# Kernel tuning notes

Hardware: AMD Instinct MI355X
Metric: run time of the kernel (lower is better)

## Reference

```python
import jax, jax.numpy as jnp
import numpy as np

N = 50000          # num nodes
E = 800000         # num edges (before self-loops)
F_IN = 128         # num_node_features
HEADS = 8          # num_heads (layer 1)
F_HEAD = 16        # features_per_head
N_CLASSES = 32     # num_classes (layer 2, heads=1)
NEG_SLOPE = 0.2    # PyG GATConv default LeakyReLU slope


def setup_inputs() -> dict:
    key = jax.random.key(0)
    ks = jax.random.split(key, 9)
    x = jax.random.normal(ks[0], (N, F_IN), jnp.float32)
    src = jax.random.randint(ks[1], (E,), 0, N, dtype=jnp.int32)
    dst = jax.random.randint(ks[2], (E,), 0, N, dtype=jnp.int32)
    # layer 1 params
    W1 = jax.random.normal(ks[3], (F_IN, HEADS * F_HEAD), jnp.float32) / np.sqrt(F_IN).astype(np.float32)
    a_src1 = jax.random.normal(ks[4], (HEADS, F_HEAD), jnp.float32) * 0.1
    a_dst1 = jax.random.normal(ks[5], (HEADS, F_HEAD), jnp.float32) * 0.1
    b1 = jnp.zeros((HEADS * F_HEAD,), jnp.float32)  # bias_init = zeros_
    # layer 2 params (heads=1)
    W2 = jax.random.normal(ks[6], (HEADS * F_HEAD, N_CLASSES), jnp.float32) / np.sqrt(HEADS * F_HEAD).astype(np.float32)
    a_src2 = jax.random.normal(ks[7], (1, N_CLASSES), jnp.float32) * 0.1
    a_dst2 = jax.random.normal(ks[8], (1, N_CLASSES), jnp.float32) * 0.1
    b2 = jnp.zeros((N_CLASSES,), jnp.float32)
    return {"x": x, "src": src, "dst": dst,
            "W1": W1, "a_src1": a_src1, "a_dst1": a_dst1, "b1": b1,
            "W2": W2, "a_src2": a_src2, "a_dst2": a_dst2, "b2": b2}


def gat_conv(x, src, dst, W, a_src, a_dst, b, heads, feat):
    """PyG-style GATConv (concat=True, add_self_loops=True)."""
    h = (x @ W).reshape(N, heads, feat)                 # [N,H,F]
    al_src = jnp.sum(h * a_src, axis=-1)                # [N,H]
    al_dst = jnp.sum(h * a_dst, axis=-1)                # [N,H]
    loop = jnp.arange(N, dtype=src.dtype)
    s = jnp.concatenate([src, loop])                    # [E+N]
    d = jnp.concatenate([dst, loop])                    # [E+N]
    e = jax.nn.leaky_relu(al_src[s] + al_dst[d], NEG_SLOPE)   # [E+N,H]
    # numerically stable softmax over edges grouped by dst node
    m = jax.ops.segment_max(e, d, num_segments=N)       # [N,H]
    ex = jnp.exp(e - m[d])
    denom = jax.ops.segment_sum(ex, d, num_segments=N)  # [N,H]
    alpha = ex / denom[d]                               # [E+N,H]
    out = jax.ops.segment_sum(alpha[:, :, None] * h[s], d, num_segments=N)  # [N,H,F]
    return out.reshape(N, heads * feat) + b


def reference(x, src, dst, W1, a_src1, a_dst1, b1, W2, a_src2, a_dst2, b2):
    h = gat_conv(x, src, dst, W1, a_src1, a_dst1, b1, HEADS, F_HEAD)
    h = jax.nn.elu(h)
    h = gat_conv(h, src, dst, W2, a_src2, a_dst2, b2, 1, N_CLASSES)
    return jax.nn.log_softmax(h, axis=1)
```

## Files before the change

kernel.cpp:

```cpp
#include <hip/hip_runtime.h>

#define N_NODES   50000
#define N_EDGES   800000
#define NEG_SLOPE 0.2f
#define NBKT      256
#define NPB       196
#define EPB       3125

__device__ __forceinline__ float leaky(float x) {
    return x > 0.f ? x : x * NEG_SLOPE;
}

__device__ __forceinline__ unsigned short f2bf(float f) {
    unsigned int u = __float_as_uint(f);
    unsigned int r = (u + 0x7FFFu + ((u >> 16) & 1u)) >> 16;
    return (unsigned short)r;
}

__device__ __forceinline__ float2 bf2f2(unsigned int p) {
    return make_float2(__uint_as_float(p << 16),
                       __uint_as_float(p & 0xFFFF0000u));
}

__device__ __forceinline__ void fma4(float4& acc, const float4 a,
                                     const float4 w0, const float4 w1,
                                     const float4 w2, const float4 w3) {
    acc.x = fmaf(a.x, w0.x, fmaf(a.y, w1.x, fmaf(a.z, w2.x, fmaf(a.w, w3.x, acc.x))));
    acc.y = fmaf(a.x, w0.y, fmaf(a.y, w1.y, fmaf(a.z, w2.y, fmaf(a.w, w3.y, acc.y))));
    acc.z = fmaf(a.x, w0.z, fmaf(a.y, w1.z, fmaf(a.z, w2.z, fmaf(a.w, w3.z, acc.z))));
    acc.w = fmaf(a.x, w0.w, fmaf(a.y, w1.w, fmaf(a.z, w2.w, fmaf(a.w, w3.w, acc.w))));
}

__device__ __forceinline__ float dot4(const float4 a, const float4 b) {
    return a.x * b.x + a.y * b.y + a.z * b.z + a.w * b.w;
}

__global__ __launch_bounds__(256) void k_hist(const int* __restrict__ dst,
                                              int* __restrict__ hist_g) {
    __shared__ int h[NBKT];
    const int tid = threadIdx.x, blk = blockIdx.x;
    h[tid] = 0;
    __syncthreads();
    const int e0 = blk * EPB;
    for (int j = e0 + tid; j < e0 + EPB; j += 256)
        atomicAdd(&h[dst[j] / NPB], 1);
    __syncthreads();
    hist_g[tid * NBKT + blk] = h[tid];
}

__global__ __launch_bounds__(256) void k_scanA(const int* __restrict__ hist_g,
                                               int* __restrict__ offs,
                                               int* __restrict__ totals) {
    __shared__ int sc[256];
    const int b = blockIdx.x, tid = threadIdx.x;
    int v = hist_g[b * 256 + tid];
    sc[tid] = v;
    __syncthreads();
    for (int off = 1; off < 256; off <<= 1) {
        int add = (tid >= off) ? sc[tid - off] : 0;
        __syncthreads();
        sc[tid] += add;
        __syncthreads();
    }
    offs[b * 256 + tid] = sc[tid] - v;
    if (tid == 255) totals[b] = sc[255];
}

__global__ __launch_bounds__(256) void k_bin_gemm1(
    const int* __restrict__ src, const int* __restrict__ dst,
    const int* __restrict__ offs, const int* __restrict__ totals,
    unsigned int* __restrict__ binned,
    const float* __restrict__ x, const float* __restrict__ W1,
    const float* __restrict__ a_src, const float* __restrict__ a_dst,
    unsigned short* __restrict__ h1b, float* __restrict__ al_src,
    float* __restrict__ al_dst)
{
    __shared__ __align__(16) unsigned char smem[65536];
    const int tid = threadIdx.x;

    if (blockIdx.x < NBKT) {
        int* cur = (int*)smem;
        int* sc  = (int*)(smem + 1024);
        const int blk = blockIdx.x;
        const int tv = totals[tid];
        sc[tid] = tv;
        __syncthreads();
        for (int off = 1; off < 256; off <<= 1) {
            int add = (tid >= off) ? sc[tid - off] : 0;
            __syncthreads();
            sc[tid] += add;
            __syncthreads();
        }
        cur[tid] = (sc[tid] - tv) + offs[tid * NBKT + blk];
        __syncthreads();
        const int e0 = blk * EPB;
        for (int j = e0 + tid; j < e0 + EPB; j += 256) {
            int d   = dst[j];
            int bkt = d / NPB;
            int dl  = d - bkt * NPB;
            int pos = atomicAdd(&cur[bkt], 1);
            binned[pos] = (unsigned int)src[j] | ((unsigned int)dl << 18);
        }
        return;
    }

    float4* xs4 = (float4*)smem;
    float4* ws4 = (float4*)(smem + 32768);
    const int bid  = (int)blockIdx.x - NBKT;
    const int half = bid & 1;
    const int row0 = (bid >> 1) * 64;
    const int tc   = tid & 15;
    const int tr   = tid >> 4;
    const float4* x4  = (const float4*)x;
    const float4* W14 = (const float4*)W1;

    #pragma unroll
    for (int p = 0; p < 8; ++p) {
        int i = tid + p * 256;
        int k = i >> 4, c4 = i & 15;
        ws4[k * 16 + c4] = W14[k * 32 + half * 16 + c4];
    }
    #pragma unroll
    for (int p = 0; p < 8; ++p) {
        int i = tid + p * 256;
        int r = i >> 5, k4 = i & 31;
        int gr = row0 + r; if (gr > N_NODES - 1) gr = N_NODES - 1;
        xs4[r * 32 + (k4 ^ ((r >> 2) & 7))] = x4[gr * 32 + k4];
    }
    __syncthreads();

    float4 acc[4];
    #pragma unroll
    for (int i = 0; i < 4; ++i) acc[i] = make_float4(0.f, 0.f, 0.f, 0.f);
    const int sw = tr & 7;
    #pragma unroll 2
    for (int k4 = 0; k4 < 32; ++k4) {
        float4 w0 = ws4[(4 * k4 + 0) * 16 + tc];
        float4 w1 = ws4[(4 * k4 + 1) * 16 + tc];
        float4 w2 = ws4[(4 * k4 + 2) * 16 + tc];
        float4 w3 = ws4[(4 * k4 + 3) * 16 + tc];
        const int kk = k4 ^ sw;
        #pragma unroll
        for (int i = 0; i < 4; ++i) {
            float4 a = xs4[(4 * tr + i) * 32 + kk];
            fma4(acc[i], a, w0, w1, w2, w3);
        }
    }

    const int c0   = half * 64 + 4 * tc;
    const int head = c0 >> 4;
    const float4 as4 = ((const float4*)a_src)[half * 16 + tc];
    const float4 ad4 = ((const float4*)a_dst)[half * 16 + tc];
    #pragma unroll
    for (int i = 0; i < 4; ++i) {
        int r = row0 + 4 * tr + i;
        if (r < N_NODES) {
            ((ushort4*)h1b)[r * 32 + half * 16 + tc] =
                make_ushort4(f2bf(acc[i].x), f2bf(acc[i].y),
                             f2bf(acc[i].z), f2bf(acc[i].w));
            float s = dot4(acc[i], as4);
            float d = dot4(acc[i], ad4);
            s += __shfl_xor(s, 1); s += __shfl_xor(s, 2);
            d += __shfl_xor(d, 1); d += __shfl_xor(d, 2);
            if ((tc & 3) == 0) {
                al_src[r * 8 + head] = s;
                al_dst[r * 8 + head] = d;
            }
        }
    }
}

__global__ __launch_bounds__(256) void k_csr_fine(const unsigned int* __restrict__ binned,
                                                  const int* __restrict__ totals,
                                                  int* __restrict__ row_ptr,
                                                  int* __restrict__ csr) {
    __shared__ int cnt[256];
    __shared__ int sc[256];
    __shared__ int cur[256];
    const int b = blockIdx.x, tid = threadIdx.x;
    sc[tid] = totals[tid];
    __syncthreads();
    for (int off = 1; off < 256; off <<= 1) {
        int add = (tid >= off) ? sc[tid - off] : 0;
        __syncthreads();
        sc[tid] += add;
        __syncthreads();
    }
    const int start = (b == 0) ? 0 : sc[b - 1];
    const int end   = sc[b];
    cnt[tid] = 0;
    __syncthreads();
    for (int j = start + tid; j < end; j += 256)
        atomicAdd(&cnt[(binned[j] >> 18) & 255], 1);
    __syncthreads();
    const int v = cnt[tid];
    sc[tid] = v;
    __syncthreads();
    for (int off = 1; off < 256; off <<= 1) {
        int add = (tid >= off) ? sc[tid - off] : 0;
        __syncthreads();
        sc[tid] += add;
        __syncthreads();
    }
    const int excl = sc[tid] - v;
    cur[tid] = excl;
    const int node = b * NPB + tid;
    if (tid < NPB && node < N_NODES) row_ptr[node] = start + excl;
    if (b == NBKT - 1 && tid == 0)   row_ptr[N_NODES] = N_EDGES;
    __syncthreads();
    for (int j = start + tid; j < end; j += 256) {
        unsigned int p = binned[j];
        int dl  = (p >> 18) & 255;
        int pos = start + atomicAdd(&cur[dl], 1);
        csr[pos] = (int)(p & 0x3FFFFu);
    }
}

__global__ __launch_bounds__(256) void k_agg1(
    const unsigned short* __restrict__ h1b, const float* __restrict__ al_src,
    const float* __restrict__ al_dst, const int* __restrict__ row_ptr,
    const int* __restrict__ csr_src, const float* __restrict__ b1,
    float* __restrict__ h2)
{
    const int n = blockIdx.x * 4 + (threadIdx.x >> 6);
    const int l    = threadIdx.x & 63;
    const int slot = l >> 4;
    const int f2   = l & 15;
    const int head = f2 >> 1;
    const uint4* h1q = (const uint4*)h1b;

    const float alD = al_dst[n * 8 + head];
    float denom = 0.f;
    float acc[8];
    #pragma unroll
    for (int i = 0; i < 8; ++i) acc[i] = 0.f;

    if (slot == 0) {
        float w = __expf(leaky(al_src[n * 8 + head] + alD));
        uint4 q = h1q[n * 16 + f2];
        float2 v0 = bf2f2(q.x), v1 = bf2f2(q.y), v2 = bf2f2(q.z), v3 = bf2f2(q.w);
        denom = w;
        acc[0] = w * v0.x; acc[1] = w * v0.y; acc[2] = w * v1.x; acc[3] = w * v1.y;
        acc[4] = w * v2.x; acc[5] = w * v2.y; acc[6] = w * v3.x; acc[7] = w * v3.y;
    }

    const int beg = row_ptr[n], end = row_ptr[n + 1];
    int j = beg + slot;
    for (; j + 12 < end; j += 16) {
        int s0 = csr_src[j];
        int s1 = csr_src[j + 4];
        int s2 = csr_src[j + 8];
        int s3 = csr_src[j + 12];
        float al0 = al_src[s0 * 8 + head];
        float al1 = al_src[s1 * 8 + head];
        float al2 = al_src[s2 * 8 + head];
        float al3 = al_src[s3 * 8 + head];
        uint4 q0 = h1q[s0 * 16 + f2];
        uint4 q1 = h1q[s1 * 16 + f2];
        uint4 q2 = h1q[s2 * 16 + f2];
        uint4 q3 = h1q[s3 * 16 + f2];
        float w0 = __expf(leaky(al0 + alD));
        float w1 = __expf(leaky(al1 + alD));
        float w2 = __expf(leaky(al2 + alD));
        float w3 = __expf(leaky(al3 + alD));
        denom += (w0 + w1) + (w2 + w3);
        float2 v;
        v = bf2f2(q0.x); acc[0] = fmaf(w0, v.x, acc[0]); acc[1] = fmaf(w0, v.y, acc[1]);
        v = bf2f2(q0.y); acc[2] = fmaf(w0, v.x, acc[2]); acc[3] = fmaf(w0, v.y, acc[3]);
        v = bf2f2(q0.z); acc[4] = fmaf(w0, v.x, acc[4]); acc[5] = fmaf(w0, v.y, acc[5]);
        v = bf2f2(q0.w); acc[6] = fmaf(w0, v.x, acc[6]); acc[7] = fmaf(w0, v.y, acc[7]);
        v = bf2f2(q1.x); acc[0] = fmaf(w1, v.x, acc[0]); acc[1] = fmaf(w1, v.y, acc[1]);
        v = bf2f2(q1.y); acc[2] = fmaf(w1, v.x, acc[2]); acc[3] = fmaf(w1, v.y, acc[3]);
        v = bf2f2(q1.z); acc[4] = fmaf(w1, v.x, acc[4]); acc[5] = fmaf(w1, v.y, acc[5]);
        v = bf2f2(q1.w); acc[6] = fmaf(w1, v.x, acc[6]); acc[7] = fmaf(w1, v.y, acc[7]);
        v = bf2f2(q2.x); acc[0] = fmaf(w2, v.x, acc[0]); acc[1] = fmaf(w2, v.y, acc[1]);
        v = bf2f2(q2.y); acc[2] = fmaf(w2, v.x, acc[2]); acc[3] = fmaf(w2, v.y, acc[3]);
        v = bf2f2(q2.z); acc[4] = fmaf(w2, v.x, acc[4]); acc[5] = fmaf(w2, v.y, acc[5]);
        v = bf2f2(q2.w); acc[6] = fmaf(w2, v.x, acc[6]); acc[7] = fmaf(w2, v.y, acc[7]);
        v = bf2f2(q3.x); acc[0] = fmaf(w3, v.x, acc[0]); acc[1] = fmaf(w3, v.y, acc[1]);
        v = bf2f2(q3.y); acc[2] = fmaf(w3, v.x, acc[2]); acc[3] = fmaf(w3, v.y, acc[3]);
        v = bf2f2(q3.z); acc[4] = fmaf(w3, v.x, acc[4]); acc[5] = fmaf(w3, v.y, acc[5]);
        v = bf2f2(q3.w); acc[6] = fmaf(w3, v.x, acc[6]); acc[7] = fmaf(w3, v.y, acc[7]);
    }
    for (; j + 4 < end; j += 8) {
        int sa = csr_src[j];
        int sb = csr_src[j + 4];
        float ala = al_src[sa * 8 + head];
        float alb = al_src[sb * 8 + head];
        uint4 qa = h1q[sa * 16 + f2];
        uint4 qb = h1q[sb * 16 + f2];
        float wa = __expf(leaky(ala + alD));
        float wb = __expf(leaky(alb + alD));
        denom += wa + wb;
        float2 v;
        v = bf2f2(qa.x); acc[0] = fmaf(wa, v.x, acc[0]); acc[1] = fmaf(wa, v.y, acc[1]);
        v = bf2f2(qa.y); acc[2] = fmaf(wa, v.x, acc[2]); acc[3] = fmaf(wa, v.y, acc[3]);
        v = bf2f2(qa.z); acc[4] = fmaf(wa, v.x, acc[4]); acc[5] = fmaf(wa, v.y, acc[5]);
        v = bf2f2(qa.w); acc[6] = fmaf(wa, v.x, acc[6]); acc[7] = fmaf(wa, v.y, acc[7]);
        v = bf2f2(qb.x); acc[0] = fmaf(wb, v.x, acc[0]); acc[1] = fmaf(wb, v.y, acc[1]);
        v = bf2f2(qb.y); acc[2] = fmaf(wb, v.x, acc[2]); acc[3] = fmaf(wb, v.y, acc[3]);
        v = bf2f2(qb.z); acc[4] = fmaf(wb, v.x, acc[4]); acc[5] = fmaf(wb, v.y, acc[5]);
        v = bf2f2(qb.w); acc[6] = fmaf(wb, v.x, acc[6]); acc[7] = fmaf(wb, v.y, acc[7]);
    }
    if (j < end) {
        int s = csr_src[j];
        float w = __expf(leaky(al_src[s * 8 + head] + alD));
        uint4 q = h1q[s * 16 + f2];
        denom += w;
        float2 v;
        v = bf2f2(q.x); acc[0] = fmaf(w, v.x, acc[0]); acc[1] = fmaf(w, v.y, acc[1]);
        v = bf2f2(q.y); acc[2] = fmaf(w, v.x, acc[2]); acc[3] = fmaf(w, v.y, acc[3]);
        v = bf2f2(q.z); acc[4] = fmaf(w, v.x, acc[4]); acc[5] = fmaf(w, v.y, acc[5]);
        v = bf2f2(q.w); acc[6] = fmaf(w, v.x, acc[6]); acc[7] = fmaf(w, v.y, acc[7]);
    }

    #pragma unroll
    for (int i = 0; i < 8; ++i) {
        acc[i] += __shfl_xor(acc[i], 16);
        acc[i] += __shfl_xor(acc[i], 32);
    }
    denom += __shfl_xor(denom, 16);
    denom += __shfl_xor(denom, 32);

    if (slot == 0) {
        const float4 bA = ((const float4*)b1)[f2 * 2];
        const float4 bB = ((const float4*)b1)[f2 * 2 + 1];
        float inv = 1.f / denom;
        float o[8];
        o[0] = acc[0] * inv + bA.x; o[1] = acc[1] * inv + bA.y;
        o[2] = acc[2] * inv + bA.z; o[3] = acc[3] * inv + bA.w;
        o[4] = acc[4] * inv + bB.x; o[5] = acc[5] * inv + bB.y;
        o[6] = acc[6] * inv + bB.z; o[7] = acc[7] * inv + bB.w;
        #pragma unroll
        for (int i = 0; i < 8; ++i) o[i] = o[i] > 0.f ? o[i] : expm1f(o[i]);
        ((float4*)h2)[n * 32 + f2 * 2]     = make_float4(o[0], o[1], o[2], o[3]);
        ((float4*)h2)[n * 32 + f2 * 2 + 1] = make_float4(o[4], o[5], o[6], o[7]);
    }
}

__global__ __launch_bounds__(128) void k_gemm2(
    const float* __restrict__ h2, const float* __restrict__ W2,
    const float* __restrict__ a_src, const float* __restrict__ a_dst,
    unsigned short* __restrict__ t2b, float* __restrict__ al_src,
    float* __restrict__ al_dst)
{
    __shared__ float4 xs4[64 * 32];
    __shared__ float4 ws4[128 * 8];
    const int tid  = threadIdx.x;
    const int row0 = (int)blockIdx.x * 64;
    const int tc   = tid & 7;
    const int tr   = tid >> 3;
    const float4* h24 = (const float4*)h2;
    const float4* W24 = (const float4*)W2;

    #pragma unroll
    for (int p = 0; p < 8; ++p) {
        int i = tid + p * 128;
        ws4[i] = W24[i];
    }
    #pragma unroll
    for (int p = 0; p < 16; ++p) {
        int i = tid + p * 128;
        int r = i >> 5, k4 = i & 31;
        int gr = row0 + r; if (gr > N_NODES - 1) gr = N_NODES - 1;
        xs4[r * 32 + (k4 ^ ((r >> 2) & 7))] = h24[gr * 32 + k4];
    }
    __syncthreads();

    float4 acc[4];
    #pragma unroll
    for (int i = 0; i < 4; ++i) acc[i] = make_float4(0.f, 0.f, 0.f, 0.f);
    const int sw = tr & 7;
    #pragma unroll 2
    for (int k4 = 0; k4 < 32; ++k4) {
        float4 w0 = ws4[(4 * k4 + 0) * 8 + tc];
        float4 w1 = ws4[(4 * k4 + 1) * 8 + tc];
        float4 w2 = ws4[(4 * k4 + 2) * 8 + tc];
        float4 w3 = ws4[(4 * k4 + 3) * 8 + tc];
        const int kk = k4 ^ sw;
        #pragma unroll
        for (int i = 0; i < 4; ++i) {
            float4 a = xs4[(4 * tr + i) * 32 + kk];
            fma4(acc[i], a, w0, w1, w2, w3);
        }
    }

    const float4 as4 = ((const float4*)a_src)[tc];
    const float4 ad4 = ((const float4*)a_dst)[tc];
    #pragma unroll
    for (int i = 0; i < 4; ++i) {
        int r = row0 + 4 * tr + i;
        if (r < N_NODES) {
            ((ushort4*)t2b)[r * 8 + tc] =
                make_ushort4(f2bf(acc[i].x), f2bf(acc[i].y),
                             f2bf(acc[i].z), f2bf(acc[i].w));
            float s = dot4(acc[i], as4);
            float d = dot4(acc[i], ad4);
            s += __shfl_xor(s, 1); s += __shfl_xor(s, 2); s += __shfl_xor(s, 4);
            d += __shfl_xor(d, 1); d += __shfl_xor(d, 2); d += __shfl_xor(d, 4);
            if (tc == 0) {
                al_src[r] = s;
                al_dst[r] = d;
            }
        }
    }
}

__global__ __launch_bounds__(256) void k_agg2(
    const unsigned short* __restrict__ t2b, const float* __restrict__ al_src,
    const float* __restrict__ al_dst, const int* __restrict__ row_ptr,
    const int* __restrict__ csr_src, const float* __restrict__ b2,
    float* __restrict__ out)
{
    const int n = blockIdx.x * 4 + (threadIdx.x >> 6);
    const int l = threadIdx.x & 63;
    const int slot = l >> 3;
    const int f4   = l & 7;
    const uint2* t2u = (const uint2*)t2b;

    const float alD = al_dst[n];
    float denom = 0.f;
    float4 acc = make_float4(0.f, 0.f, 0.f, 0.f);
    if (slot == 0) {
        float w = __expf(leaky(al_src[n] + alD));
        uint2 q = t2u[n * 8 + f4];
        float2 v0 = bf2f2(q.x), v1 = bf2f2(q.y);
        denom = w;
        acc = make_float4(w * v0.x, w * v0.y, w * v1.x, w * v1.y);
    }
    const int beg = row_ptr[n], end = row_ptr[n + 1];
    int j = beg + slot;
    for (; j + 8 < end; j += 16) {
        int sa = csr_src[j];
        int sb = csr_src[j + 8];
        float ala = al_src[sa];
        float alb = al_src[sb];
        uint2 qa = t2u[sa * 8 + f4];
        uint2 qb = t2u[sb * 8 + f4];
        float wa = __expf(leaky(ala + alD));
        float wb = __expf(leaky(alb + alD));
        denom += wa + wb;
        float2 v;
        v = bf2f2(qa.x); acc.x = fmaf(wa, v.x, acc.x); acc.y = fmaf(wa, v.y, acc.y);
        v = bf2f2(qa.y); acc.z = fmaf(wa, v.x, acc.z); acc.w = fmaf(wa, v.y, acc.w);
        v = bf2f2(qb.x); acc.x = fmaf(wb, v.x, acc.x); acc.y = fmaf(wb, v.y, acc.y);
        v = bf2f2(qb.y); acc.z = fmaf(wb, v.x, acc.z); acc.w = fmaf(wb, v.y, acc.w);
    }
    if (j < end) {
        int s = csr_src[j];
        float w = __expf(leaky(al_src[s] + alD));
        uint2 q = t2u[s * 8 + f4];
        denom += w;
        float2 v;
        v = bf2f2(q.x); acc.x = fmaf(w, v.x, acc.x); acc.y = fmaf(w, v.y, acc.y);
        v = bf2f2(q.y); acc.z = fmaf(w, v.x, acc.z); acc.w = fmaf(w, v.y, acc.w);
    }
    #pragma unroll
    for (int off = 8; off <= 32; off <<= 1) {
        acc.x += __shfl_xor(acc.x, off); acc.y += __shfl_xor(acc.y, off);
        acc.z += __shfl_xor(acc.z, off); acc.w += __shfl_xor(acc.w, off);
        denom += __shfl_xor(denom, off);
    }

    const float4 bb = ((const float4*)b2)[f4];
    float inv = 1.f / denom;
    float o0 = acc.x * inv + bb.x;
    float o1 = acc.y * inv + bb.y;
    float o2 = acc.z * inv + bb.z;
    float o3 = acc.w * inv + bb.w;
    float m = fmaxf(fmaxf(o0, o1), fmaxf(o2, o3));
    for (int off = 1; off <= 4; off <<= 1) m = fmaxf(m, __shfl_xor(m, off));
    float ssum = __expf(o0 - m) + __expf(o1 - m) + __expf(o2 - m) + __expf(o3 - m);
    for (int off = 1; off <= 4; off <<= 1) ssum += __shfl_xor(ssum, off);
    float lg = m + __logf(ssum);
    if (slot == 0)
        ((float4*)out)[n * 8 + f4] = make_float4(o0 - lg, o1 - lg, o2 - lg, o3 - lg);
}

extern "C" void kernel_launch(void* const* d_in, const int* in_sizes, int n_in,
                              void* d_out, int out_size, void* d_ws, size_t ws_size,
                              hipStream_t stream) {
    const float* x      = (const float*)d_in[0];
    const int*   src    = (const int*)d_in[1];
    const int*   dst    = (const int*)d_in[2];
    const float* W1     = (const float*)d_in[3];
    const float* a_src1 = (const float*)d_in[4];
    const float* a_dst1 = (const float*)d_in[5];
    const float* b1     = (const float*)d_in[6];
    const float* W2     = (const float*)d_in[7];
    const float* a_src2 = (const float*)d_in[8];
    const float* a_dst2 = (const float*)d_in[9];
    const float* b2     = (const float*)d_in[10];
    float* out = (float*)d_out;

    char* ws = (char*)d_ws;
    size_t off = 0;
    auto alloc = [&](size_t bytes) {
        void* p = ws + off;
        off += (bytes + 255) & ~(size_t)255;
        return p;
    };
    unsigned short* h1b = (unsigned short*)alloc((size_t)N_NODES * 128 * 2);
    float*          h2  = (float*)alloc((size_t)N_NODES * 128 * 4);
    unsigned short* t2b = (unsigned short*)alloc((size_t)N_NODES * 32 * 2);
    float* alS1    = (float*)alloc((size_t)N_NODES * 8 * 4);
    float* alD1    = (float*)alloc((size_t)N_NODES * 8 * 4);
    float* alS2    = (float*)alloc((size_t)N_NODES * 4);
    float* alD2    = (float*)alloc((size_t)N_NODES * 4);
    int*   rowp    = (int*)alloc((size_t)(N_NODES + 1) * 4);
    int*   csr     = (int*)alloc((size_t)N_EDGES * 4);
    unsigned int* binned = (unsigned int*)alloc((size_t)N_EDGES * 4);
    int*   hist_g  = (int*)alloc((size_t)NBKT * NBKT * 4);
    int*   offs    = (int*)alloc((size_t)NBKT * NBKT * 4);
    int*   totals  = (int*)alloc((size_t)NBKT * 4);
    (void)ws_size; (void)in_sizes; (void)n_in; (void)out_size;

    const int row_tiles = (N_NODES + 63) / 64;

    k_hist<<<NBKT, 256, 0, stream>>>(dst, hist_g);
    k_scanA<<<NBKT, 256, 0, stream>>>(hist_g, offs, totals);
    k_bin_gemm1<<<NBKT + row_tiles * 2, 256, 0, stream>>>(
        src, dst, offs, totals, binned,
        x, W1, a_src1, a_dst1, h1b, alS1, alD1);
    k_csr_fine<<<NBKT, 256, 0, stream>>>(binned, totals, rowp, csr);
    k_agg1<<<N_NODES / 4, 256, 0, stream>>>(h1b, alS1, alD1, rowp, csr, b1, h2);
    k_gemm2<<<row_tiles, 128, 0, stream>>>(h2, W2, a_src2, a_dst2, t2b, alS2, alD2);
    k_agg2<<<N_NODES / 4, 256, 0, stream>>>(t2b, alS2, alD2, rowp, csr, b2, out);
}
```

Measured before the change: 223.6 us.

## Replace histogram-scan binning with fixed-capacity buckets and global atomic cursors

Drops the separate histogram and scan kernels. Each binning block now counts its edges per bucket in shared memory and reserves space with one global atomicAdd per bucket into fixed-capacity slots of CAP entries. Because buckets are no longer packed, the CSR uses separate row_beg/row_end arrays. The change also removes the 4-way unrolled edge loop in k_agg1. This saves two launches and a pass over dst, but silently overflows if any bucket gets more than 4096 edges, and the shorter unroll in agg1 may reduce memory-level parallelism.

```diff
diff --git a/kernel.cpp b/kernel.cpp
--- a/kernel.cpp
+++ b/kernel.cpp
@@ -6,6 +6,7 @@
 #define NBKT      256
 #define NPB       196
 #define EPB       3125
+#define CAP       4096
 
 __device__ __forceinline__ float leaky(float x) {
     return x > 0.f ? x : x * NEG_SLOPE;
@@ -35,41 +36,9 @@
     return a.x * b.x + a.y * b.y + a.z * b.z + a.w * b.w;
 }
 
-__global__ __launch_bounds__(256) void k_hist(const int* __restrict__ dst,
-                                              int* __restrict__ hist_g) {
-    __shared__ int h[NBKT];
-    const int tid = threadIdx.x, blk = blockIdx.x;
-    h[tid] = 0;
-    __syncthreads();
-    const int e0 = blk * EPB;
-    for (int j = e0 + tid; j < e0 + EPB; j += 256)
-        atomicAdd(&h[dst[j] / NPB], 1);
-    __syncthreads();
-    hist_g[tid * NBKT + blk] = h[tid];
-}
-
-__global__ __launch_bounds__(256) void k_scanA(const int* __restrict__ hist_g,
-                                               int* __restrict__ offs,
-                                               int* __restrict__ totals) {
-    __shared__ int sc[256];
-    const int b = blockIdx.x, tid = threadIdx.x;
-    int v = hist_g[b * 256 + tid];
-    sc[tid] = v;
-    __syncthreads();
-    for (int off = 1; off < 256; off <<= 1) {
-        int add = (tid >= off) ? sc[tid - off] : 0;
-        __syncthreads();
-        sc[tid] += add;
-        __syncthreads();
-    }
-    offs[b * 256 + tid] = sc[tid] - v;
-    if (tid == 255) totals[b] = sc[255];
-}
-
 __global__ __launch_bounds__(256) void k_bin_gemm1(
     const int* __restrict__ src, const int* __restrict__ dst,
-    const int* __restrict__ offs, const int* __restrict__ totals,
-    unsigned int* __restrict__ binned,
+    int* __restrict__ cursor_g, unsigned int* __restrict__ binned,
     const float* __restrict__ x, const float* __restrict__ W1,
     const float* __restrict__ a_src, const float* __restrict__ a_dst,
     unsigned short* __restrict__ h1b, float* __restrict__ al_src,
@@ -79,27 +48,28 @@
     const int tid = threadIdx.x;
 
     if (blockIdx.x < NBKT) {
-        int* cur = (int*)smem;
-        int* sc  = (int*)(smem + 1024);
+        int* dstc = (int*)smem;
+        int* cnt  = (int*)(smem + 12512);
+        int* cur  = (int*)(smem + 13536);
         const int blk = blockIdx.x;
-        const int tv = totals[tid];
-        sc[tid] = tv;
+        const int e0  = blk * EPB;
+        cnt[tid] = 0;
         __syncthreads();
-        for (int off = 1; off < 256; off <<= 1) {
-            int add = (tid >= off) ? sc[tid - off] : 0;
-            __syncthreads();
-            sc[tid] += add;
-            __syncthreads();
-        }
-        cur[tid] = (sc[tid] - tv) + offs[tid * NBKT + blk];
+        for (int j = tid; j < EPB; j += 256) {
+            int d = dst[e0 + j];
+            dstc[j] = d;
+            atomicAdd(&cnt[d / NPB], 1);
+        }
         __syncthreads();
-        const int e0 = blk * EPB;
-        for (int j = e0 + tid; j < e0 + EPB; j += 256) {
-            int d   = dst[j];
+        int base = atomicAdd(&cursor_g[tid], cnt[tid]);
+        cur[tid] = tid * CAP + base;
+        __syncthreads();
+        for (int j = tid; j < EPB; j += 256) {
+            int d   = dstc[j];
             int bkt = d / NPB;
             int dl  = d - bkt * NPB;
             int pos = atomicAdd(&cur[bkt], 1);
-            binned[pos] = (unsigned int)src[j] | ((unsigned int)dl << 18);
+            binned[pos] = (unsigned int)src[e0 + j] | ((unsigned int)dl << 18);
         }
         return;
     }
@@ -171,14 +141,23 @@
 }
 
 __global__ __launch_bounds__(256) void k_csr_fine(const unsigned int* __restrict__ binned,
-                                                  const int* __restrict__ totals,
-                                                  int* __restrict__ row_ptr,
+                                                  const int* __restrict__ cursor_g,
+                                                  int* __restrict__ row_beg,
+                                                  int* __restrict__ row_end,
                                                   int* __restrict__ csr) {
     __shared__ int cnt[256];
     __shared__ int sc[256];
     __shared__ int cur[256];
     const int b = blockIdx.x, tid = threadIdx.x;
-    sc[tid] = totals[tid];
+    const int start = b * CAP;
+    const int nE    = cursor_g[b];
+    cnt[tid] = 0;
+    __syncthreads();
+    for (int j = tid; j < nE; j += 256)
+        atomicAdd(&cnt[(binned[start + j] >> 18) & 255], 1);
+    __syncthreads();
+    const int v = cnt[tid];
+    sc[tid] = v;
     __syncthreads();
     for (int off = 1; off < 256; off <<= 1) {
         int add = (tid >= off) ? sc[tid - off] : 0;
@@ -186,30 +165,16 @@
         sc[tid] += add;
         __syncthreads();
     }
-    const int start = (b == 0) ? 0 : sc[b - 1];
-    const int end   = sc[b];
-    cnt[tid] = 0;
-    __syncthreads();
-    for (int j = start + tid; j < end; j += 256)
-        atomicAdd(&cnt[(binned[j] >> 18) & 255], 1);
-    __syncthreads();
-    const int v = cnt[tid];
-    sc[tid] = v;
-    __syncthreads();
-    for (int off = 1; off < 256; off <<= 1) {
-        int add = (tid >= off) ? sc[tid - off] : 0;
-        __syncthreads();
-        sc[tid] += add;
-        __syncthreads();
-    }
     const int excl = sc[tid] - v;
     cur[tid] = excl;
     const int node = b * NPB + tid;
-    if (tid < NPB && node < N_NODES) row_ptr[node] = start + excl;
-    if (b == NBKT - 1 && tid == 0)   row_ptr[N_NODES] = N_EDGES;
-    __syncthreads();
-    for (int j = start + tid; j < end; j += 256) {
-        unsigned int p = binned[j];
+    if (tid < NPB && node < N_NODES) {
+        row_beg[node] = start + excl;
+        row_end[node] = start + excl + v;
+    }
+    __syncthreads();
+    for (int j = tid; j < nE; j += 256) {
+        unsigned int p = binned[start + j];
         int dl  = (p >> 18) & 255;
         int pos = start + atomicAdd(&cur[dl], 1);
         csr[pos] = (int)(p & 0x3FFFFu);
@@ -218,9 +183,9 @@
 
 __global__ __launch_bounds__(256) void k_agg1(
     const unsigned short* __restrict__ h1b, const float* __restrict__ al_src,
-    const float* __restrict__ al_dst, const int* __restrict__ row_ptr,
-    const int* __restrict__ csr_src, const float* __restrict__ b1,
-    float* __restrict__ h2)
+    const float* __restrict__ al_dst, const int* __restrict__ row_beg,
+    const int* __restrict__ row_end, const int* __restrict__ csr_src,
+    const float* __restrict__ b1, float* __restrict__ h2)
 {
     const int n = blockIdx.x * 4 + (threadIdx.x >> 6);
     const int l    = threadIdx.x & 63;
@@ -244,44 +209,8 @@
         acc[4] = w * v2.x; acc[5] = w * v2.y; acc[6] = w * v3.x; acc[7] = w * v3.y;
     }
 
-    const int beg = row_ptr[n], end = row_ptr[n + 1];
+    const int beg = row_beg[n], end = row_end[n];
     int j = beg + slot;
-    for (; j + 12 < end; j += 16) {
-        int s0 = csr_src[j];
-        int s1 = csr_src[j + 4];
-        int s2 = csr_src[j + 8];
-        int s3 = csr_src[j + 12];
-        float al0 = al_src[s0 * 8 + head];
-        float al1 = al_src[s1 * 8 + head];
-        float al2 = al_src[s2 * 8 + head];
-        float al3 = al_src[s3 * 8 + head];
-        uint4 q0 = h1q[s0 * 16 + f2];
-        uint4 q1 = h1q[s1 * 16 + f2];
-        uint4 q2 = h1q[s2 * 16 + f2];
-        uint4 q3 = h1q[s3 * 16 + f2];
-        float w0 = __expf(leaky(al0 + alD));
-        float w1 = __expf(leaky(al1 + alD));
-        float w2 = __expf(leaky(al2 + alD));
-        float w3 = __expf(leaky(al3 + alD));
-        denom += (w0 + w1) + (w2 + w3);
-        float2 v;
-        v = bf2f2(q0.x); acc[0] = fmaf(w0, v.x, acc[0]); acc[1] = fmaf(w0, v.y, acc[1]);
-        v = bf2f2(q0.y); acc[2] = fmaf(w0, v.x, acc[2]); acc[3] = fmaf(w0, v.y, acc[3]);
-        v = bf2f2(q0.z); acc[4] = fmaf(w0, v.x, acc[4]); acc[5] = fmaf(w0, v.y, acc[5]);
-        v = bf2f2(q0.w); acc[6] = fmaf(w0, v.x, acc[6]); acc[7] = fmaf(w0, v.y, acc[7]);
-        v = bf2f2(q1.x); acc[0] = fmaf(w1, v.x, acc[0]); acc[1] = fmaf(w1, v.y, acc[1]);
-        v = bf2f2(q1.y); acc[2] = fmaf(w1, v.x, acc[2]); acc[3] = fmaf(w1, v.y, acc[3]);
-        v = bf2f2(q1.z); acc[4] = fmaf(w1, v.x, acc[4]); acc[5] = fmaf(w1, v.y, acc[5]);
-        v = bf2f2(q1.w); acc[6] = fmaf(w1, v.x, acc[6]); acc[7] = fmaf(w1, v.y, acc[7]);
-        v = bf2f2(q2.x); acc[0] = fmaf(w2, v.x, acc[0]); acc[1] = fmaf(w2, v.y, acc[1]);
-        v = bf2f2(q2.y); acc[2] = fmaf(w2, v.x, acc[2]); acc[3] = fmaf(w2, v.y, acc[3]);
-        v = bf2f2(q2.z); acc[4] = fmaf(w2, v.x, acc[4]); acc[5] = fmaf(w2, v.y, acc[5]);
-        v = bf2f2(q2.w); acc[6] = fmaf(w2, v.x, acc[6]); acc[7] = fmaf(w2, v.y, acc[7]);
-        v = bf2f2(q3.x); acc[0] = fmaf(w3, v.x, acc[0]); acc[1] = fmaf(w3, v.y, acc[1]);
-        v = bf2f2(q3.y); acc[2] = fmaf(w3, v.x, acc[2]); acc[3] = fmaf(w3, v.y, acc[3]);
-        v = bf2f2(q3.z); acc[4] = fmaf(w3, v.x, acc[4]); acc[5] = fmaf(w3, v.y, acc[5]);
-        v = bf2f2(q3.w); acc[6] = fmaf(w3, v.x, acc[6]); acc[7] = fmaf(w3, v.y, acc[7]);
-    }
     for (; j + 4 < end; j += 8) {
         int sa = csr_src[j];
         int sb = csr_src[j + 4];
@@ -408,9 +337,9 @@
 
 __global__ __launch_bounds__(256) void k_agg2(
     const unsigned short* __restrict__ t2b, const float* __restrict__ al_src,
-    const float* __restrict__ al_dst, const int* __restrict__ row_ptr,
-    const int* __restrict__ csr_src, const float* __restrict__ b2,
-    float* __restrict__ out)
+    const float* __restrict__ al_dst, const int* __restrict__ row_beg,
+    const int* __restrict__ row_end, const int* __restrict__ csr_src,
+    const float* __restrict__ b2, float* __restrict__ out)
 {
     const int n = blockIdx.x * 4 + (threadIdx.x >> 6);
     const int l = threadIdx.x & 63;
@@ -428,7 +357,7 @@
         denom = w;
         acc = make_float4(w * v0.x, w * v0.y, w * v1.x, w * v1.y);
     }
-    const int beg = row_ptr[n], end = row_ptr[n + 1];
+    const int beg = row_beg[n], end = row_end[n];
     int j = beg + slot;
     for (; j + 8 < end; j += 16) {
         int sa = csr_src[j];
@@ -507,23 +436,21 @@
     float* alD1    = (float*)alloc((size_t)N_NODES * 8 * 4);
     float* alS2    = (float*)alloc((size_t)N_NODES * 4);
     float* alD2    = (float*)alloc((size_t)N_NODES * 4);
-    int*   rowp    = (int*)alloc((size_t)(N_NODES + 1) * 4);
-    int*   csr     = (int*)alloc((size_t)N_EDGES * 4);
-    unsigned int* binned = (unsigned int*)alloc((size_t)N_EDGES * 4);
-    int*   hist_g  = (int*)alloc((size_t)NBKT * NBKT * 4);
-    int*   offs    = (int*)alloc((size_t)NBKT * NBKT * 4);
-    int*   totals  = (int*)alloc((size_t)NBKT * 4);
+    int*   row_beg = (int*)alloc((size_t)N_NODES * 4);
+    int*   row_end = (int*)alloc((size_t)N_NODES * 4);
+    int*   csr     = (int*)alloc((size_t)NBKT * CAP * 4);
+    unsigned int* binned = (unsigned int*)alloc((size_t)NBKT * CAP * 4);
+    int*   cursor  = (int*)alloc((size_t)NBKT * 4);
     (void)ws_size; (void)in_sizes; (void)n_in; (void)out_size;
 
     const int row_tiles = (N_NODES + 63) / 64;
 
-    k_hist<<<NBKT, 256, 0, stream>>>(dst, hist_g);
-    k_scanA<<<NBKT, 256, 0, stream>>>(hist_g, offs, totals);
+    hipMemsetAsync(cursor, 0, (size_t)NBKT * 4, stream);
     k_bin_gemm1<<<NBKT + row_tiles * 2, 256, 0, stream>>>(
-        src, dst, offs, totals, binned,
+        src, dst, cursor, binned,
         x, W1, a_src1, a_dst1, h1b, alS1, alD1);
-    k_csr_fine<<<NBKT, 256, 0, stream>>>(binned, totals, rowp, csr);
-    k_agg1<<<N_NODES / 4, 256, 0, stream>>>(h1b, alS1, alD1, rowp, csr, b1, h2);
+    k_csr_fine<<<NBKT, 256, 0, stream>>>(binned, cursor, row_beg, row_end, csr);
+    k_agg1<<<N_NODES / 4, 256, 0, stream>>>(h1b, alS1, alD1, row_beg, row_end, csr, b1, h2);
     k_gemm2<<<row_tiles, 128, 0, stream>>>(h2, W2, a_src2, a_dst2, t2b, alS2, alD2);
-    k_agg2<<<N_NODES / 4, 256, 0, stream>>>(t2b, alS2, alD2, rowp, csr, b2, out);
-}
+    k_agg2<<<N_NODES / 4, 256, 0, stream>>>(t2b, alS2, alD2, row_beg, row_end, csr, b2, out);
+}
```

Result: faster. 218.2 us (-2.4%).
